# Kernel tuning notes

Hardware: AMD Instinct MI355X
Metric: run time of the kernel (lower is better)

Reference implementation:

```python
import jax, jax.numpy as jnp
import numpy as np

B, S, D, H = 2, 2048, 1024, 16
DK = D // H

def setup_inputs() -> dict:
    key = jax.random.key(0)
    ks = jax.random.split(key, 5)
    scale = 1.0 / np.sqrt(D)
    return {
        "x": jax.random.normal(ks[0], (B, S, D), dtype=jnp.float32),
        "W_qkv": jax.random.uniform(ks[1], (D, 3 * D), dtype=jnp.float32, minval=-scale, maxval=scale),
        "b_qkv": jax.random.uniform(ks[2], (3 * D,), dtype=jnp.float32, minval=-scale, maxval=scale),
        "W_o": jax.random.uniform(ks[3], (D, D), dtype=jnp.float32, minval=-scale, maxval=scale),
        "b_o": jax.random.uniform(ks[4], (D,), dtype=jnp.float32, minval=-scale, maxval=scale),
    }

def reference(x, W_qkv, b_qkv, W_o, b_o):
    # fused QKV projection: [B,S,3D] -> [B,S,H,3*dk]
    qkv = (x @ W_qkv + b_qkv).reshape(B, S, H, 3 * DK)
    q, k, v = qkv[..., :DK], qkv[..., DK:2 * DK], qkv[..., 2 * DK:]
    # scores [B,H,S,S]; note: original module's masked_fill is a discarded no-op, so no mask applied
    a = jnp.einsum("bqhd,bkhd->bhqk", q, k) / np.sqrt(DK).astype(np.float32)
    a = jax.nn.softmax(a, axis=-1)
    o = jnp.einsum("bhqk,bkhd->bqhd", a, v).reshape(B, S, D)
    return o @ W_o + b_o
```

## Files before the change

### kernel.cpp

```cpp
#include <hip/hip_runtime.h>
#include <hip/hip_bf16.h>

typedef __bf16 bf16;
typedef __attribute__((ext_vector_type(8))) __bf16 bf16x8;
typedef __attribute__((ext_vector_type(4))) __bf16 bf16x4;
typedef __attribute__((ext_vector_type(4))) float f32x4;
typedef __attribute__((ext_vector_type(16))) float f32x16;
typedef __attribute__((ext_vector_type(4))) unsigned int u32x4;
typedef __attribute__((ext_vector_type(2))) unsigned int u32x2;

#define DEV static __device__ __forceinline__

DEV f32x4 mfma16(bf16x8 a, bf16x8 b, f32x4 c) {
  return __builtin_amdgcn_mfma_f32_16x16x32_bf16(a, b, c, 0, 0, 0);
}
DEV f32x16 mfma32(bf16x8 a, bf16x8 b, f32x16 c) {
  return __builtin_amdgcn_mfma_f32_32x32x16_bf16(a, b, c, 0, 0, 0);
}
DEV unsigned int pk2(float a, float b) {
  unsigned short ua = __builtin_bit_cast(unsigned short, (bf16)a);
  unsigned short ub = __builtin_bit_cast(unsigned short, (bf16)b);
  return ((unsigned int)ub << 16) | ua;
}
DEV void gload16(const void* g, void* l) {
  __builtin_amdgcn_global_load_lds(
      (const __attribute__((address_space(1))) unsigned int*)g,
      (__attribute__((address_space(3))) unsigned int*)l, 16, 0, 0);
}
DEV u32x2 xhalf(unsigned int a, unsigned int b, int hi) {
#if __has_builtin(__builtin_amdgcn_permlane32_swap)
  return __builtin_amdgcn_permlane32_swap(a, b, false, false);
#else
  unsigned int xa = __shfl_xor(a, 32), xb = __shfl_xor(b, 32);
  u32x2 r;
  r.x = hi ? xb : a;
  r.y = hi ? b : xa;
  return r;
#endif
}


__global__ __launch_bounds__(256) void prep_k(
    const float* __restrict__ x, bf16* __restrict__ xb,
    const float* __restrict__ wqkv, bf16* __restrict__ wqkvT,
    const float* __restrict__ wo, bf16* __restrict__ woT) {
  __shared__ bf16 ts[64][68];
  const int tid = threadIdx.x;
  const int bid = blockIdx.x;
  if (bid < 2048) {
    int gid = bid * 256 + tid;
    const float* src = x + (size_t)gid * 8;
    f32x4 a0 = *(const f32x4*)src;
    f32x4 a1 = *(const f32x4*)(src + 4);
    bf16x8 pk;
#pragma unroll
    for (int j = 0; j < 4; ++j) { pk[j] = (bf16)a0[j]; pk[j + 4] = (bf16)a1[j]; }
    *(bf16x8*)(xb + (size_t)gid * 8) = pk;
    return;
  }
  const float* w;
  bf16* wt;
  int N, K, n0, k0;
  if (bid < 2816) {
    int r = bid - 2048;
    w = wqkv; wt = wqkvT; N = 3072; K = 1024;
    n0 = (r % 48) * 64; k0 = (r / 48) * 64;
  } else {
    int r = bid - 2816;
    w = wo; wt = woT; N = 1024; K = 1024;
    n0 = (r % 16) * 64; k0 = (r / 16) * 64;
  }
  const int tr = tid >> 4;
  const int tc = (tid & 15) * 4;
#pragma unroll
  for (int p = 0; p < 4; ++p) {
    int kr = p * 16 + tr;
    f32x4 v = *(const f32x4*)(w + (size_t)(k0 + kr) * N + n0 + tc);
#pragma unroll
    for (int j = 0; j < 4; ++j) ts[tc + j][kr] = (bf16)v[j];
  }
  __syncthreads();
#pragma unroll
  for (int p = 0; p < 4; ++p) {
    int nr = p * 16 + tr;
    bf16x4 o4;
#pragma unroll
    for (int j = 0; j < 4; ++j) o4[j] = ts[nr][tc + j];
    *(bf16x4*)(wt + (size_t)(n0 + nr) * K + k0 + tc) = o4;
  }
}

__global__ __launch_bounds__(256, 2) void qkv_gemm_k(
    const bf16* __restrict__ xb, const bf16* __restrict__ wt,
    const float* __restrict__ bias,
    bf16* __restrict__ qo, bf16* __restrict__ ko, bf16* __restrict__ vt) {
  __shared__ __align__(16) char As[16384];
  __shared__ __align__(16) char Bs[16384];
  const int tid = threadIdx.x;
  const int lane = tid & 63;
  const int wid = tid >> 6;
  const int wm = wid >> 1, wn = wid & 1;
  const int l16 = lane & 15, lhi = lane >> 4;
  const int m0 = blockIdx.y * 128;
  const int n0 = blockIdx.x * 128;
  const char* ap = (const char*)xb;
  const char* bp = (const char*)wt;

  f32x4 acc[4][4] = {};

  for (int kt = 0; kt < 1024; kt += 64) {
#pragma unroll
    for (int i = 0; i < 4; ++i) {
      int n = i * 256 + wid * 64 + lane;
      int row = n >> 3, c16 = n & 7;
      gload16(ap + (size_t)(m0 + row) * 2048 + kt * 2 + ((c16 * 16) ^ ((row & 7) << 4)),
              As + (i * 256 + wid * 64) * 16);
    }
#pragma unroll
    for (int i = 0; i < 4; ++i) {
      int n = i * 256 + wid * 64 + lane;
      int row = n >> 3, c16 = n & 7;
      gload16(bp + (size_t)(n0 + row) * 2048 + kt * 2 + ((c16 * 16) ^ ((row & 7) << 4)),
              Bs + (i * 256 + wid * 64) * 16);
    }
    __syncthreads();
#pragma unroll
    for (int kc = 0; kc < 2; ++kc) {
      bf16x8 af[4], bfr[4];
#pragma unroll
      for (int ii = 0; ii < 4; ++ii) {
        int row = wm * 64 + ii * 16 + l16;
        af[ii] = *(const bf16x8*)(As + row * 128 +
                                  ((kc * 64 + lhi * 16) ^ ((row & 7) << 4)));
      }
#pragma unroll
      for (int jj = 0; jj < 4; ++jj) {
        int n = wn * 64 + jj * 16 + l16;
        bfr[jj] = *(const bf16x8*)(Bs + n * 128 +
                                   ((kc * 64 + lhi * 16) ^ ((n & 7) << 4)));
      }
#pragma unroll
      for (int ii = 0; ii < 4; ++ii)
#pragma unroll
        for (int jj = 0; jj < 4; ++jj)
          acc[ii][jj] = mfma16(af[ii], bfr[jj], acc[ii][jj]);
    }
    __syncthreads();
  }

  const float SCQ = 0.18033688011112042f;
#pragma unroll
  for (int jj = 0; jj < 4; ++jj) {
    int nbase = n0 + wn * 64 + jj * 16;
    int h = nbase / 192;
    int rem = nbase - h * 192;
    int type = rem >> 6;
    int dk0 = rem & 63;
    float bv = bias[nbase + l16];
    if (type < 2) {
      bf16* dst = (type == 0) ? qo : ko;
      float scl = (type == 0) ? SCQ : 1.0f;
#pragma unroll
      for (int ii = 0; ii < 4; ++ii) {
#pragma unroll
        for (int r = 0; r < 4; ++r) {
          int mrow = m0 + wm * 64 + ii * 16 + lhi * 4 + r;
          int b = mrow >> 11, s = mrow & 2047;
          dst[(size_t)((b * 16 + h) * 2048 + s) * 64 + dk0 + l16] =
              (bf16)((acc[ii][jj][r] + bv) * scl);
        }
      }
    } else {
#pragma unroll
      for (int ii = 0; ii < 4; ++ii) {
        int s0 = m0 + wm * 64 + ii * 16 + lhi * 4;
        int b = s0 >> 11, s = s0 & 2047;
        bf16x4 w4;
#pragma unroll
        for (int r = 0; r < 4; ++r) w4[r] = (bf16)(acc[ii][jj][r] + bv);
        *(bf16x4*)(vt + (size_t)((b * 16 + h) * 64 + dk0 + l16) * 2048 + s) = w4;
      }
    }
  }
}

__global__ __launch_bounds__(256, 4) void attn_k(
    const bf16* __restrict__ q, const bf16* __restrict__ k,
    const bf16* __restrict__ vt, bf16* __restrict__ opart,
    float* __restrict__ lpart) {
  __shared__ __align__(16) char Ks[2][8192];
  __shared__ __align__(16) char Vs[2][8192];
  const int tid = threadIdx.x;
  const int lane = tid & 63;
  const int wid = tid >> 6;
  const int l31 = lane & 31;
  const int hi = lane >> 5;
  const int bh = blockIdx.x;
  const int half = blockIdx.z;
  const bf16* qp = q + (size_t)bh * 2048 * 64;
  const char* kp = (const char*)(k + (size_t)bh * 2048 * 64);
  const char* vp = (const char*)(vt + (size_t)bh * 64 * 2048);
  const int q0 = blockIdx.y * 128 + wid * 32;
  const int kv0 = half * 512;

  bf16x8 qf[4];
#pragma unroll
  for (int c = 0; c < 4; ++c)
    qf[c] = *(const bf16x8*)(qp + (size_t)(q0 + l31) * 64 + c * 16 + 8 * hi);

  f32x16 ot0 = {}, ot1 = {};
  float l_ = 0.f;

  auto STAGE = [&](int kt, int bs) {
#pragma unroll
    for (int i = 0; i < 2; ++i) {
      int n = i * 256 + wid * 64 + lane;
      int row = n >> 3, c16 = n & 7;
      const char* src = kp + (size_t)(kt + row) * 128 + ((c16 * 16) ^ ((row & 7) << 4));
      gload16(src, Ks[bs] + (i * 256 + wid * 64) * 16);
    }
#pragma unroll
    for (int i = 0; i < 2; ++i) {
      int n = i * 256 + wid * 64 + lane;
      int row = n >> 3, c16 = n & 7;
      const char* src = vp + (size_t)row * 4096 + (size_t)kt * 2 +
                        ((c16 * 16) ^ ((row & 7) << 4));
      gload16(src, Vs[bs] + (i * 256 + wid * 64) * 16);
    }
  };

  STAGE(kv0, 0);
  __syncthreads();

  for (int t = 0; t < 8; ++t) {
    int bs = t & 1;
    if (t < 7) STAGE(kv0 + (t + 1) * 64, bs ^ 1);

    float p[2][16];
#pragma unroll
    for (int kb = 0; kb < 2; ++kb) {
      bf16x8 kf[4];
#pragma unroll
      for (int c = 0; c < 4; ++c) {
        int row = kb * 32 + l31;
        kf[c] = *(const bf16x8*)(Ks[bs] + row * 128 +
                                 ((c * 32 + 16 * hi) ^ ((row & 7) << 4)));
      }
      f32x16 st = {};
      __builtin_amdgcn_s_setprio(1);
#pragma unroll
      for (int c = 0; c < 4; ++c) st = mfma32(kf[c], qf[c], st);
      __builtin_amdgcn_s_setprio(0);
#pragma unroll
      for (int r = 0; r < 16; ++r) {
        p[kb][r] = __builtin_amdgcn_exp2f(st[r]);
        l_ += p[kb][r];
      }
    }

#pragma unroll
    for (int ch = 0; ch < 4; ++ch) {
      const int kb = ch >> 1, off = (ch & 1) * 8;
      unsigned int w0 = pk2(p[kb][off + 0], p[kb][off + 1]);
      unsigned int w1 = pk2(p[kb][off + 2], p[kb][off + 3]);
      unsigned int w2 = pk2(p[kb][off + 4], p[kb][off + 5]);
      unsigned int w3 = pk2(p[kb][off + 6], p[kb][off + 7]);
      u32x2 s02 = xhalf(w0, w2, hi);
      u32x2 s13 = xhalf(w1, w3, hi);
      u32x4 ww;
      ww.x = s02.x;
      ww.y = s13.x;
      ww.z = s02.y;
      ww.w = s13.y;
      bf16x8 pb = __builtin_bit_cast(bf16x8, ww);
      int col = ch * 32 + 16 * hi;
      int r0 = l31, r1 = 32 + l31;
      bf16x8 vf0 = *(const bf16x8*)(Vs[bs] + r0 * 128 + (col ^ ((r0 & 7) << 4)));
      bf16x8 vf1 = *(const bf16x8*)(Vs[bs] + r1 * 128 + (col ^ ((r1 & 7) << 4)));
      __builtin_amdgcn_s_setprio(1);
      ot0 = mfma32(vf0, pb, ot0);
      ot1 = mfma32(vf1, pb, ot1);
      __builtin_amdgcn_s_setprio(0);
    }
    __syncthreads();
  }

  float lt = l_ + __shfl_xor(l_, 32);
  if (hi == 0) lpart[(size_t)(half * 32 + bh) * 2048 + q0 + l31] = lt;

  char* scr = &Ks[0][0] + wid * 4096;
  {
    int sw = (l31 & 7) << 4;
#pragma unroll
    for (int g = 0; g < 4; ++g) {
      bf16x4 v0, v1;
#pragma unroll
      for (int j = 0; j < 4; ++j) {
        v0[j] = (bf16)ot0[g * 4 + j];
        v1[j] = (bf16)ot1[g * 4 + j];
      }
      *(bf16x4*)(scr + l31 * 128 + ((g * 16) ^ sw) + 8 * hi) = v0;
      *(bf16x4*)(scr + l31 * 128 + (((4 + g) * 16) ^ sw) + 8 * hi) = v1;
    }
  }
  char* obase = (char*)(opart + ((size_t)(half * 32 + bh) * 2048 + q0) * 64);
#pragma unroll
  for (int p = 0; p < 4; ++p) {
    int row = p * 8 + (lane >> 3);
    int gran = lane & 7;
    u32x4 v = *(const u32x4*)(scr + row * 128 + ((gran * 16) ^ ((row & 7) << 4)));
    *(u32x4*)(obase + row * 128 + gran * 16) = v;
  }
}

__global__ __launch_bounds__(256) void comb_k(const bf16* __restrict__ opart,
                                              const float* __restrict__ lpart,
                                              bf16* __restrict__ o) {
  const size_t HS = 32ull * 2048 * 64;
  int gid = blockIdx.x * 256 + threadIdx.x;
  int dq = gid & 15;
  int s = (gid >> 4) & 2047;
  int bh = gid >> 15;
  size_t i0 = ((size_t)bh * 2048 + s) * 64 + dq * 4;
  float l = 0.f;
#pragma unroll
  for (int sp = 0; sp < 4; ++sp) l += lpart[(size_t)(sp * 32 + bh) * 2048 + s];
  f32x4 acc = {};
#pragma unroll
  for (int sp = 0; sp < 4; ++sp) {
    bf16x4 v = *(const bf16x4*)(opart + sp * HS + i0);
#pragma unroll
    for (int j = 0; j < 4; ++j) acc[j] += (float)v[j];
  }
  float inv = 1.f / l;
  int b = bh >> 4, h = bh & 15;
  bf16x4 r;
#pragma unroll
  for (int j = 0; j < 4; ++j) r[j] = (bf16)(acc[j] * inv);
  *(bf16x4*)(o + (size_t)(b * 2048 + s) * 1024 + h * 64 + dq * 4) = r;
}

__global__ __launch_bounds__(256, 2) void out_gemm_k(
    const bf16* __restrict__ a, const bf16* __restrict__ wt,
    const float* __restrict__ bias, float* __restrict__ out) {
  __shared__ __align__(16) char As[16384];
  __shared__ __align__(16) char Bs[16384];
  const int tid = threadIdx.x;
  const int lane = tid & 63;
  const int wid = tid >> 6;
  const int wm = wid >> 1, wn = wid & 1;
  const int l16 = lane & 15, lhi = lane >> 4;
  const int m0 = blockIdx.y * 128;
  const int n0 = blockIdx.x * 128;
  const char* ap = (const char*)a;
  const char* bp = (const char*)wt;

  f32x4 acc[4][4] = {};

  for (int kt = 0; kt < 1024; kt += 64) {
#pragma unroll
    for (int i = 0; i < 4; ++i) {
      int n = i * 256 + wid * 64 + lane;
      int row = n >> 3, c16 = n & 7;
      gload16(ap + (size_t)(m0 + row) * 2048 + kt * 2 + ((c16 * 16) ^ ((row & 7) << 4)),
              As + (i * 256 + wid * 64) * 16);
    }
#pragma unroll
    for (int i = 0; i < 4; ++i) {
      int n = i * 256 + wid * 64 + lane;
      int row = n >> 3, c16 = n & 7;
      gload16(bp + (size_t)(n0 + row) * 2048 + kt * 2 + ((c16 * 16) ^ ((row & 7) << 4)),
              Bs + (i * 256 + wid * 64) * 16);
    }
    __syncthreads();
#pragma unroll
    for (int kc = 0; kc < 2; ++kc) {
      bf16x8 af[4], bfr[4];
#pragma unroll
      for (int ii = 0; ii < 4; ++ii) {
        int row = wm * 64 + ii * 16 + l16;
        af[ii] = *(const bf16x8*)(As + row * 128 +
                                  ((kc * 64 + lhi * 16) ^ ((row & 7) << 4)));
      }
#pragma unroll
      for (int jj = 0; jj < 4; ++jj) {
        int n = wn * 64 + jj * 16 + l16;
        bfr[jj] = *(const bf16x8*)(Bs + n * 128 +
                                   ((kc * 64 + lhi * 16) ^ ((n & 7) << 4)));
      }
#pragma unroll
      for (int ii = 0; ii < 4; ++ii)
#pragma unroll
        for (int jj = 0; jj < 4; ++jj)
          acc[ii][jj] = mfma16(af[ii], bfr[jj], acc[ii][jj]);
    }
    __syncthreads();
  }

#pragma unroll
  for (int jj = 0; jj < 4; ++jj) {
    int nbase = n0 + wn * 64 + jj * 16;
    float bv = bias[nbase + l16];
#pragma unroll
    for (int ii = 0; ii < 4; ++ii) {
#pragma unroll
      for (int r = 0; r < 4; ++r) {
        int mrow = m0 + wm * 64 + ii * 16 + lhi * 4 + r;
        out[(size_t)mrow * 1024 + nbase + l16] = acc[ii][jj][r] + bv;
      }
    }
  }
}

extern "C" void kernel_launch(void* const* d_in, const int* in_sizes, int n_in,
                              void* d_out, int out_size, void* d_ws, size_t ws_size,
                              hipStream_t stream) {
  const float* x = (const float*)d_in[0];
  const float* wqkv = (const float*)d_in[1];
  const float* bqkv = (const float*)d_in[2];
  const float* wo = (const float*)d_in[3];
  const float* bo = (const float*)d_in[4];
  float* out = (float*)d_out;

  bf16* qws = (bf16*)d_ws;
  bf16* kws = qws + 4194304;
  bf16* vtws = kws + 4194304;
  bf16* ows = vtws + 4194304;
  bf16* wqkvT = ows + 4194304;
  bf16* woT = wqkvT + 3145728;
  bf16* opart = woT + 1048576;
  float* lpart = (float*)(opart + 16777216);
  bf16* xbf = opart;

  prep_k<<<3072, 256, 0, stream>>>(x, xbf, wqkv, wqkvT, wo, woT);
  qkv_gemm_k<<<dim3(24, 32), 256, 0, stream>>>(xbf, wqkvT, bqkv, qws, kws, vtws);
  attn_k<<<dim3(32, 16, 4), 256, 0, stream>>>(qws, kws, vtws, opart, lpart);
  comb_k<<<4096, 256, 0, stream>>>(opart, lpart, ows);
  out_gemm_k<<<dim3(8, 32), 256, 0, stream>>>(ows, woT, bo, out);
}
```

Measured before the change: 123.1 us.

## Fuse split-KV combine into attention block and shrink output GEMM N-tile

The attention kernel now runs 512-thread blocks where two groups of four waves each process half of the KV range. The halves are merged in LDS with the normalization applied in-kernel, which removes the separate combine kernel and the partial-output and partial-sum workspace traffic. The output projection GEMM uses 64-wide N tiles, doubling its grid to 512 blocks for better CU coverage. In exchange, each attention block holds 64 KB of LDS, which may lower occupancy, and the GEMM reuses each A tile less.

```diff
diff --git a/kernel.cpp b/kernel.cpp
--- a/kernel.cpp
+++ b/kernel.cpp
@@ -184,24 +184,26 @@
   }
 }
 
-__global__ __launch_bounds__(256, 4) void attn_k(
+__global__ __launch_bounds__(512, 4) void attn_k(
     const bf16* __restrict__ q, const bf16* __restrict__ k,
-    const bf16* __restrict__ vt, bf16* __restrict__ opart,
-    float* __restrict__ lpart) {
-  __shared__ __align__(16) char Ks[2][8192];
-  __shared__ __align__(16) char Vs[2][8192];
+    const bf16* __restrict__ vt, bf16* __restrict__ o) {
+  __shared__ __align__(16) char lds[65536];
   const int tid = threadIdx.x;
   const int lane = tid & 63;
   const int wid = tid >> 6;
+  const int half = wid >> 2;
+  const int wv = wid & 3;
   const int l31 = lane & 31;
   const int hi = lane >> 5;
   const int bh = blockIdx.x;
-  const int half = blockIdx.z;
+  const int b = bh >> 4, h = bh & 15;
   const bf16* qp = q + (size_t)bh * 2048 * 64;
   const char* kp = (const char*)(k + (size_t)bh * 2048 * 64);
   const char* vp = (const char*)(vt + (size_t)bh * 64 * 2048);
-  const int q0 = blockIdx.y * 128 + wid * 32;
-  const int kv0 = half * 512;
+  const int q0 = blockIdx.y * 128 + wv * 32;
+  const int kv0 = half * 1024;
+  char* myK = lds + half * 32768;
+  char* myV = lds + half * 32768 + 16384;
 
   bf16x8 qf[4];
 #pragma unroll
@@ -209,33 +211,27 @@
     qf[c] = *(const bf16x8*)(qp + (size_t)(q0 + l31) * 64 + c * 16 + 8 * hi);
 
   f32x16 ot0 = {}, ot1 = {};
-  float l_ = 0.f;
+  float la = 0.f, lb = 0.f;
 
   auto STAGE = [&](int kt, int bs) {
 #pragma unroll
     for (int i = 0; i < 2; ++i) {
-      int n = i * 256 + wid * 64 + lane;
-      int row = n >> 3, c16 = n & 7;
-      const char* src = kp + (size_t)(kt + row) * 128 + ((c16 * 16) ^ ((row & 7) << 4));
-      gload16(src, Ks[bs] + (i * 256 + wid * 64) * 16);
+      int n = i * 256 + wv * 64 + lane;
+      int row = n >> 3, c16 = n & 7;
+      gload16(kp + (size_t)(kt + row) * 128 + ((c16 * 16) ^ ((row & 7) << 4)),
+              myK + bs * 8192 + n * 16);
     }
 #pragma unroll
     for (int i = 0; i < 2; ++i) {
-      int n = i * 256 + wid * 64 + lane;
-      int row = n >> 3, c16 = n & 7;
-      const char* src = vp + (size_t)row * 4096 + (size_t)kt * 2 +
-                        ((c16 * 16) ^ ((row & 7) << 4));
-      gload16(src, Vs[bs] + (i * 256 + wid * 64) * 16);
+      int n = i * 256 + wv * 64 + lane;
+      int row = n >> 3, c16 = n & 7;
+      gload16(vp + (size_t)row * 4096 + (size_t)kt * 2 + ((c16 * 16) ^ ((row & 7) << 4)),
+              myV + bs * 8192 + n * 16);
     }
   };
 
-  STAGE(kv0, 0);
-  __syncthreads();
-
-  for (int t = 0; t < 8; ++t) {
-    int bs = t & 1;
-    if (t < 7) STAGE(kv0 + (t + 1) * 64, bs ^ 1);
-
+  auto TILE = [&](int bs, int ktn) {
+    if (ktn >= 0) STAGE(ktn, bs ^ 1);
     float p[2][16];
 #pragma unroll
     for (int kb = 0; kb < 2; ++kb) {
@@ -243,7 +239,7 @@
 #pragma unroll
       for (int c = 0; c < 4; ++c) {
         int row = kb * 32 + l31;
-        kf[c] = *(const bf16x8*)(Ks[bs] + row * 128 +
+        kf[c] = *(const bf16x8*)(myK + bs * 8192 + row * 128 +
                                  ((c * 32 + 16 * hi) ^ ((row & 7) << 4)));
       }
       f32x16 st = {};
@@ -254,10 +250,9 @@
 #pragma unroll
       for (int r = 0; r < 16; ++r) {
         p[kb][r] = __builtin_amdgcn_exp2f(st[r]);
-        l_ += p[kb][r];
-      }
-    }
-
+        if (r & 1) lb += p[kb][r]; else la += p[kb][r];
+      }
+    }
 #pragma unroll
     for (int ch = 0; ch < 4; ++ch) {
       const int kb = ch >> 1, off = (ch & 1) * 8;
@@ -275,107 +270,113 @@
       bf16x8 pb = __builtin_bit_cast(bf16x8, ww);
       int col = ch * 32 + 16 * hi;
       int r0 = l31, r1 = 32 + l31;
-      bf16x8 vf0 = *(const bf16x8*)(Vs[bs] + r0 * 128 + (col ^ ((r0 & 7) << 4)));
-      bf16x8 vf1 = *(const bf16x8*)(Vs[bs] + r1 * 128 + (col ^ ((r1 & 7) << 4)));
+      bf16x8 vf0 = *(const bf16x8*)(myV + bs * 8192 + r0 * 128 + (col ^ ((r0 & 7) << 4)));
+      bf16x8 vf1 = *(const bf16x8*)(myV + bs * 8192 + r1 * 128 + (col ^ ((r1 & 7) << 4)));
       __builtin_amdgcn_s_setprio(1);
       ot0 = mfma32(vf0, pb, ot0);
       ot1 = mfma32(vf1, pb, ot1);
       __builtin_amdgcn_s_setprio(0);
     }
     __syncthreads();
-  }
-
-  float lt = l_ + __shfl_xor(l_, 32);
-  if (hi == 0) lpart[(size_t)(half * 32 + bh) * 2048 + q0 + l31] = lt;
-
-  char* scr = &Ks[0][0] + wid * 4096;
-  {
+  };
+
+  STAGE(kv0, 0);
+  __syncthreads();
+  for (int t = 0; t < 16; t += 2) {
+    TILE(0, kv0 + (t + 1) * 64);
+    TILE(1, t + 2 < 16 ? kv0 + (t + 2) * 64 : -1);
+  }
+
+  float lt = la + lb;
+  lt += __shfl_xor(lt, 32);
+  char* cbuf = lds + 32768 + wv * 8192;
+  float* lbuf = (float*)(lds + 16384);
+  const int swl = (lane & 7) << 4;
+  if (half == 1) {
+#pragma unroll
+    for (int g = 0; g < 4; ++g) {
+      f32x4 v0, v1;
+#pragma unroll
+      for (int j = 0; j < 4; ++j) { v0[j] = ot0[g * 4 + j]; v1[j] = ot1[g * 4 + j]; }
+      *(f32x4*)(cbuf + lane * 128 + ((g * 16) ^ swl)) = v0;
+      *(f32x4*)(cbuf + lane * 128 + ((64 + g * 16) ^ swl)) = v1;
+    }
+    lbuf[wv * 64 + lane] = lt;
+  }
+  __syncthreads();
+  if (half == 0) {
+    float ltp = lbuf[wv * 64 + lane];
+    float inv = 1.f / (lt + ltp);
+#pragma unroll
+    for (int g = 0; g < 4; ++g) {
+      f32x4 a0 = *(const f32x4*)(cbuf + lane * 128 + ((g * 16) ^ swl));
+      f32x4 a1 = *(const f32x4*)(cbuf + lane * 128 + ((64 + g * 16) ^ swl));
+#pragma unroll
+      for (int j = 0; j < 4; ++j) {
+        ot0[g * 4 + j] += a0[j];
+        ot1[g * 4 + j] += a1[j];
+      }
+    }
+    char* scr = lds + wv * 4096;
     int sw = (l31 & 7) << 4;
 #pragma unroll
     for (int g = 0; g < 4; ++g) {
       bf16x4 v0, v1;
 #pragma unroll
       for (int j = 0; j < 4; ++j) {
-        v0[j] = (bf16)ot0[g * 4 + j];
-        v1[j] = (bf16)ot1[g * 4 + j];
+        v0[j] = (bf16)(ot0[g * 4 + j] * inv);
+        v1[j] = (bf16)(ot1[g * 4 + j] * inv);
       }
       *(bf16x4*)(scr + l31 * 128 + ((g * 16) ^ sw) + 8 * hi) = v0;
       *(bf16x4*)(scr + l31 * 128 + (((4 + g) * 16) ^ sw) + 8 * hi) = v1;
     }
-  }
-  char* obase = (char*)(opart + ((size_t)(half * 32 + bh) * 2048 + q0) * 64);
-#pragma unroll
-  for (int p = 0; p < 4; ++p) {
-    int row = p * 8 + (lane >> 3);
-    int gran = lane & 7;
-    u32x4 v = *(const u32x4*)(scr + row * 128 + ((gran * 16) ^ ((row & 7) << 4)));
-    *(u32x4*)(obase + row * 128 + gran * 16) = v;
-  }
-}
-
-__global__ __launch_bounds__(256) void comb_k(const bf16* __restrict__ opart,
-                                              const float* __restrict__ lpart,
-                                              bf16* __restrict__ o) {
-  const size_t HS = 32ull * 2048 * 64;
-  int gid = blockIdx.x * 256 + threadIdx.x;
-  int dq = gid & 15;
-  int s = (gid >> 4) & 2047;
-  int bh = gid >> 15;
-  size_t i0 = ((size_t)bh * 2048 + s) * 64 + dq * 4;
-  float l = 0.f;
-#pragma unroll
-  for (int sp = 0; sp < 4; ++sp) l += lpart[(size_t)(sp * 32 + bh) * 2048 + s];
-  f32x4 acc = {};
-#pragma unroll
-  for (int sp = 0; sp < 4; ++sp) {
-    bf16x4 v = *(const bf16x4*)(opart + sp * HS + i0);
-#pragma unroll
-    for (int j = 0; j < 4; ++j) acc[j] += (float)v[j];
-  }
-  float inv = 1.f / l;
-  int b = bh >> 4, h = bh & 15;
-  bf16x4 r;
-#pragma unroll
-  for (int j = 0; j < 4; ++j) r[j] = (bf16)(acc[j] * inv);
-  *(bf16x4*)(o + (size_t)(b * 2048 + s) * 1024 + h * 64 + dq * 4) = r;
+#pragma unroll
+    for (int p = 0; p < 4; ++p) {
+      int row = p * 8 + (lane >> 3);
+      int gran = lane & 7;
+      u32x4 v = *(const u32x4*)(scr + row * 128 + ((gran * 16) ^ ((row & 7) << 4)));
+      *(u32x4*)((char*)o + ((size_t)(b * 2048 + q0 + row) * 1024 + h * 64) * 2 +
+                gran * 16) = v;
+    }
+  }
 }
 
 __global__ __launch_bounds__(256, 2) void out_gemm_k(
     const bf16* __restrict__ a, const bf16* __restrict__ wt,
     const float* __restrict__ bias, float* __restrict__ out) {
   __shared__ __align__(16) char As[16384];
-  __shared__ __align__(16) char Bs[16384];
+  __shared__ __align__(16) char Bs[8192];
   const int tid = threadIdx.x;
   const int lane = tid & 63;
   const int wid = tid >> 6;
   const int wm = wid >> 1, wn = wid & 1;
   const int l16 = lane & 15, lhi = lane >> 4;
   const int m0 = blockIdx.y * 128;
-  const int n0 = blockIdx.x * 128;
+  const int n0 = blockIdx.x * 64;
   const char* ap = (const char*)a;
   const char* bp = (const char*)wt;
 
-  f32x4 acc[4][4] = {};
+  f32x4 acc[4][2] = {};
 
   for (int kt = 0; kt < 1024; kt += 64) {
 #pragma unroll
     for (int i = 0; i < 4; ++i) {
-      int n = i * 256 + wid * 64 + lane;
+      int n = i * 256 + tid;
       int row = n >> 3, c16 = n & 7;
       gload16(ap + (size_t)(m0 + row) * 2048 + kt * 2 + ((c16 * 16) ^ ((row & 7) << 4)),
-              As + (i * 256 + wid * 64) * 16);
-    }
-#pragma unroll
-    for (int i = 0; i < 4; ++i) {
-      int n = i * 256 + wid * 64 + lane;
+              As + n * 16);
+    }
+#pragma unroll
+    for (int i = 0; i < 2; ++i) {
+      int n = i * 256 + tid;
       int row = n >> 3, c16 = n & 7;
       gload16(bp + (size_t)(n0 + row) * 2048 + kt * 2 + ((c16 * 16) ^ ((row & 7) << 4)),
-              Bs + (i * 256 + wid * 64) * 16);
+              Bs + n * 16);
     }
     __syncthreads();
 #pragma unroll
     for (int kc = 0; kc < 2; ++kc) {
-      bf16x8 af[4], bfr[4];
+      bf16x8 af[4], bfr[2];
 #pragma unroll
       for (int ii = 0; ii < 4; ++ii) {
         int row = wm * 64 + ii * 16 + l16;
@@ -383,23 +384,23 @@
                                   ((kc * 64 + lhi * 16) ^ ((row & 7) << 4)));
       }
 #pragma unroll
-      for (int jj = 0; jj < 4; ++jj) {
-        int n = wn * 64 + jj * 16 + l16;
+      for (int jj = 0; jj < 2; ++jj) {
+        int n = wn * 32 + jj * 16 + l16;
         bfr[jj] = *(const bf16x8*)(Bs + n * 128 +
                                    ((kc * 64 + lhi * 16) ^ ((n & 7) << 4)));
       }
 #pragma unroll
       for (int ii = 0; ii < 4; ++ii)
 #pragma unroll
-        for (int jj = 0; jj < 4; ++jj)
+        for (int jj = 0; jj < 2; ++jj)
           acc[ii][jj] = mfma16(af[ii], bfr[jj], acc[ii][jj]);
     }
     __syncthreads();
   }
 
 #pragma unroll
-  for (int jj = 0; jj < 4; ++jj) {
-    int nbase = n0 + wn * 64 + jj * 16;
+  for (int jj = 0; jj < 2; ++jj) {
+    int nbase = n0 + wn * 32 + jj * 16;
     float bv = bias[nbase + l16];
 #pragma unroll
     for (int ii = 0; ii < 4; ++ii) {
@@ -428,13 +429,10 @@
   bf16* ows = vtws + 4194304;
   bf16* wqkvT = ows + 4194304;
   bf16* woT = wqkvT + 3145728;
-  bf16* opart = woT + 1048576;
-  float* lpart = (float*)(opart + 16777216);
-  bf16* xbf = opart;
+  bf16* xbf = woT + 1048576;
 
   prep_k<<<3072, 256, 0, stream>>>(x, xbf, wqkv, wqkvT, wo, woT);
   qkv_gemm_k<<<dim3(24, 32), 256, 0, stream>>>(xbf, wqkvT, bqkv, qws, kws, vtws);
-  attn_k<<<dim3(32, 16, 4), 256, 0, stream>>>(qws, kws, vtws, opart, lpart);
-  comb_k<<<4096, 256, 0, stream>>>(opart, lpart, ows);
-  out_gemm_k<<<dim3(8, 32), 256, 0, stream>>>(ows, woT, bo, out);
-}
+  attn_k<<<dim3(32, 16), 512, 0, stream>>>(qws, kws, vtws, ows);
+  out_gemm_k<<<dim3(16, 32), 256, 0, stream>>>(ows, woT, bo, out);
+}
```

Result: faster. 107.3 us (median of 2 runs) (-12.9%).
